# Kernel optimization log

Hardware: AMD Instinct MI355X
Metric: run time of the kernel (lower is better)

Reference implementation:

```python
import jax, jax.numpy as jnp
import numpy as np

NUM_HEADS = 6
EPS = 1e-6

def setup_inputs() -> dict:
    key = jax.random.key(0)
    k1, k2, k3, k4, k5 = jax.random.split(key, 5)
    B, N, C = 8, 1024, 384
    x = jax.random.normal(k1, (B, N, C), dtype=jnp.float32)
    # torch nn.Linear weights stored here as [in, out] for y = x @ W
    w_qkv = jax.random.normal(k2, (C, 3 * C), dtype=jnp.float32) * 0.02
    w_out = jax.random.normal(k3, (C, C), dtype=jnp.float32) * 0.02
    b_out = jax.random.normal(k4, (C,), dtype=jnp.float32) * 0.02
    # non-negative random-walk visitation mask (avg visits per node)
    mask = jax.random.uniform(k5, (N, N), dtype=jnp.float32)
    return {"x": x, "w_qkv": w_qkv, "w_out": w_out, "b_out": b_out, "mask": mask}

def reference(x, w_qkv, w_out, b_out, mask):
    B, N, C = x.shape
    H = NUM_HEADS
    D = C // H
    qkv = x @ w_qkv                                   # [B,N,3C]
    q, k, v = jnp.split(qkv, 3, axis=-1)
    # [B,N,C] -> [B,H,N,D]
    to_heads = lambda t: t.reshape(B, N, H, D).transpose(0, 2, 1, 3)
    q, k, v = to_heads(q), to_heads(k), to_heads(v)
    # feature map: relu(x) + eps
    q = jax.nn.relu(q) + EPS
    k = jax.nn.relu(k) + EPS
    # masked linear kernel: (Phi(Q) Phi(K)^T * mask)
    kernel = jnp.einsum("bhnd,bhmd->bhnm", q, k) * mask  # [B,H,N,N]
    z = 1.0 / (kernel.sum(axis=-1, keepdims=True) + EPS)  # row normalizer
    out = jnp.einsum("bhnm,bhmd->bhnd", kernel, v) * z    # [B,H,N,D]
    out = out.transpose(0, 2, 1, 3).reshape(B, N, C)
    return out @ w_out + b_out
```

## Files before the change

kernel.cpp:

```cpp
#include <hip/hip_runtime.h>
#include <hip/hip_bf16.h>
#include <hip/hip_fp16.h>
#include <stdint.h>

typedef __hip_bfloat16 bf16;
typedef __attribute__((ext_vector_type(8))) short short8;
typedef __attribute__((ext_vector_type(4))) float f32x4;
typedef __attribute__((ext_vector_type(16))) float f32x16;
typedef __attribute__((ext_vector_type(4))) int int4v;
typedef __attribute__((ext_vector_type(4))) unsigned short ushort4v;

#define MFMA16(A,B,C) __builtin_amdgcn_mfma_f32_16x16x32_bf16(A,B,C,0,0,0)
#define MFMA32(A,B,C) __builtin_amdgcn_mfma_f32_32x32x16_bf16(A,B,C,0,0,0)

#define FENCE() asm volatile("" ::: "memory")
#define SBAR()  do { FENCE(); __builtin_amdgcn_s_barrier(); FENCE(); } while (0)
#define WAITVN(N) asm volatile("s_waitcnt vmcnt(" #N ")" ::: "memory")

static __device__ __forceinline__ void g2lds16(const void* g, void* l) {
  __builtin_amdgcn_global_load_lds(
      (__attribute__((address_space(1))) void*)(g),
      (__attribute__((address_space(3))) void*)(l), 16, 0, 0);
}

static __device__ __forceinline__ int swz8(int row, int kc) {
  return row * 8 + (kc ^ (row & 7));
}

static __device__ __forceinline__ unsigned short f2bf_bits(float f) {
  bf16 t = __float2bfloat16(f); unsigned short u; __builtin_memcpy(&u, &t, 2); return u;
}
static __device__ __forceinline__ unsigned short f2h_bits(float f) {
  __half t = __float2half(f); unsigned short u; __builtin_memcpy(&u, &t, 2); return u;
}

template<bool HALFOUT>
static __device__ __forceinline__ void tileT(const float* __restrict__ in,
                                             unsigned short* __restrict__ out,
                                             int R, int C, int tr, int tc, int tid,
                                             float (*tls)[65]) {
  const int rr0 = tid >> 4, c4 = tid & 15;
  #pragma unroll
  for (int rr = 0; rr < 4; ++rr) {
    int r = rr0 + rr * 16;
    float4 v = *(const float4*)(in + (size_t)(tr * 64 + r) * C + tc * 64 + c4 * 4);
    tls[r][c4 * 4 + 0] = v.x; tls[r][c4 * 4 + 1] = v.y;
    tls[r][c4 * 4 + 2] = v.z; tls[r][c4 * 4 + 3] = v.w;
  }
  __syncthreads();
  #pragma unroll
  for (int rr = 0; rr < 4; ++rr) {
    int r2 = rr0 + rr * 16;
    ushort4v o;
    #pragma unroll
    for (int k = 0; k < 4; ++k) {
      float f = tls[c4 * 4 + k][r2];
      o[k] = HALFOUT ? f2h_bits(f) : f2bf_bits(f);
    }
    *(ushort4v*)(out + (size_t)(tc * 64 + r2) * R + tr * 64 + c4 * 4) = o;
  }
}

__global__ __launch_bounds__(256)
void k_prep(const float* __restrict__ x, bf16* __restrict__ xb,
            const float* __restrict__ wqkv, unsigned short* __restrict__ wqkvT,
            const float* __restrict__ wout, unsigned short* __restrict__ woutT,
            const float* __restrict__ mask, unsigned short* __restrict__ maskT) {
  __shared__ float tls[64][65];
  const int bid = blockIdx.x, tid = threadIdx.x;
  if (bid < 768) {
    #pragma unroll
    for (int j = 0; j < 4; ++j) {
      int i = bid * 1024 + j * 256 + tid;
      float4 v = ((const float4*)x)[i];
      bf16* po = xb + (size_t)i * 4;
      po[0] = __float2bfloat16(v.x); po[1] = __float2bfloat16(v.y);
      po[2] = __float2bfloat16(v.z); po[3] = __float2bfloat16(v.w);
    }
  } else if (bid < 876) {
    int tt = bid - 768; tileT<false>(wqkv, wqkvT, 384, 1152, tt / 18, tt % 18, tid, tls);
  } else if (bid < 912) {
    int tt = bid - 876; tileT<false>(wout, woutT, 384, 384, tt / 6, tt % 6, tid, tls);
  } else {
    int tt = bid - 912; tileT<true>(mask, maskT, 1024, 1024, tt / 16, tt % 16, tid, tls);
  }
}

__global__ __launch_bounds__(256, 3)
void k_gemm_qkv(const bf16* __restrict__ A, const bf16* __restrict__ BT,
                bf16* __restrict__ Cb, bf16* __restrict__ vT)
{
  __shared__ __align__(16) bf16 As[128 * 64];
  __shared__ __align__(16) bf16 Bs[96 * 64];
  const int tid = threadIdx.x;
  const int wave = tid >> 6, lane = tid & 63;
  const int lhi = lane >> 4, llo = lane & 15;
  const int wr = wave >> 1, wc = wave & 1;
  const int mBase = blockIdx.x * 128, nBase = blockIdx.y * 96;
  const int K = 384, N = 1152;

  f32x4 acc[4][3] = {};

  for (int kt = 0; kt < K; kt += 64) {
    __syncthreads();
    #pragma unroll
    for (int i = 0; i < 4; ++i) {
      int c = i * 256 + tid;
      int row = c >> 3;
      int kc = (c & 7) ^ (row & 7);
      g2lds16(A + (size_t)(mBase + row) * K + kt + kc * 8, As + (c & ~63) * 8);
    }
    #pragma unroll
    for (int i = 0; i < 3; ++i) {
      int c = i * 256 + tid;
      int row = c >> 3;
      int kc = (c & 7) ^ (row & 7);
      g2lds16(BT + (size_t)(nBase + row) * K + kt + kc * 8, Bs + (c & ~63) * 8);
    }
    __syncthreads();
    for (int kk = 0; kk < 2; ++kk) {
      const int kc = kk * 4 + lhi;
      short8 a[4], b[3];
      #pragma unroll
      for (int mi = 0; mi < 4; ++mi)
        a[mi] = *(const short8*)(As + swz8(wr * 64 + mi * 16 + llo, kc) * 8);
      #pragma unroll
      for (int ni = 0; ni < 3; ++ni)
        b[ni] = *(const short8*)(Bs + swz8(wc * 48 + ni * 16 + llo, kc) * 8);
      #pragma unroll
      for (int mi = 0; mi < 4; ++mi)
        #pragma unroll
        for (int ni = 0; ni < 3; ++ni)
          acc[mi][ni] = MFMA16(a[mi], b[ni], acc[mi][ni]);
    }
  }

  const bool isV = (nBase >= 768);
  #pragma unroll
  for (int mi = 0; mi < 4; ++mi)
    #pragma unroll
    for (int ni = 0; ni < 3; ++ni) {
      const int colbase = nBase + wc * 48 + ni * 16;
      if (!isV) {
        #pragma unroll
        for (int j = 0; j < 4; ++j) {
          int row = mBase + wr * 64 + mi * 16 + lhi * 4 + j;
          int col = colbase + llo;
          float v = fmaxf(acc[mi][ni][j], 0.f) + 1e-6f;
          Cb[(size_t)row * N + col] = __float2bfloat16(v);
        }
      } else {
        int col = colbase + llo;
        int dall = col - 768, hh = dall >> 6, dd = dall & 63;
        int rowg = mBase + wr * 64 + mi * 16 + lhi * 4;
        int bb = rowg >> 10, nloc = rowg & 1023;
        ushort4v pk;
        #pragma unroll
        for (int j = 0; j < 4; ++j) pk[j] = f2bf_bits(acc[mi][ni][j]);
        *(ushort4v*)((unsigned short*)vT + (((size_t)bb * 6 + hh) * 64 + dd) * 1024 + nloc) = pk;
      }
    }
}

__global__ __launch_bounds__(256, 3)
void k_attn(const bf16* __restrict__ qkv,
            const bf16* __restrict__ vT,
            const __half* __restrict__ maskT,
            bf16* __restrict__ out)
{
  __shared__ __align__(16) char smem[49664];
  bf16* KsB = (bf16*)smem;
  bf16* VsB = KsB + 3 * 4096;
  float* OredF = (float*)smem;
  float* zredF = (float*)(smem + 49152);

  const int bid = blockIdx.x;
  const int bh = bid % 48, qt = bid / 48;
  const int b = bh / 6, h = bh - b * 6;
  const int tid = threadIdx.x, wave = tid >> 6, lane = tid & 63;
  const int lq = lane & 31, lh = lane >> 5;
  const int wq = wave & 1, wm = wave >> 1;
  const size_t row0 = (size_t)b * 1024;
  const int qglob = qt * 64 + wq * 32 + lq;

  auto stageKV = [&](int mt, int buf) {
    #pragma unroll
    for (int i = 0; i < 2; ++i) {
      int c = (wave * 2 + i) * 64 + lane;
      int row = c >> 3;
      int kc = (c & 7) ^ (row & 7);
      g2lds16(qkv + (row0 + mt * 64 + row) * 1152 + 384 + h * 64 + kc * 8,
              KsB + buf * 4096 + (c & ~63) * 8);
      g2lds16(vT + ((size_t)bh * 64 + row) * 1024 + mt * 64 + kc * 8,
              VsB + buf * 4096 + (c & ~63) * 8);
    }
  };
  auto loadMask = [&](int mt, __half (&mv)[16]) {
    const int mrow0 = mt * 64 + wm * 32 + 4 * lh;
    #pragma unroll
    for (int g = 0; g < 4; ++g)
      #pragma unroll
      for (int j = 0; j < 4; ++j)
        mv[g * 4 + j] = maskT[(size_t)(mrow0 + 8 * g + j) * 1024 + qglob];
  };

  short8 bq[4];
  {
    const bf16* qp = qkv + (row0 + qglob) * 1152 + h * 64 + lh * 8;
    #pragma unroll
    for (int ks = 0; ks < 4; ++ks) bq[ks] = *(const short8*)(qp + ks * 16);
  }

  f32x16 accO[2] = {};
  float zl = 0.f;

  __half mvA[16], mvB[16];
  stageKV(0, 0);
  loadMask(0, mvA);

  auto iter = [&](int t, __half (&mvUse)[16], __half (&mvPre)[16]) {
    const int bc = t % 3;
    const bf16* Kc = KsB + bc * 4096;
    const bf16* Vc = VsB + bc * 4096;

    if (t < 15) {
      stageKV(t + 1, (t + 1) % 3);
      WAITVN(4);
    } else {
      WAITVN(0);
    }
    asm volatile("s_waitcnt lgkmcnt(0)" ::: "memory");
    SBAR();

    if (t < 15) loadMask(t + 1, mvPre);

    f32x16 st = {};
    #pragma unroll
    for (int ks = 0; ks < 4; ++ks) {
      int row = wm * 32 + lq;
      int cc = (ks * 2 + lh) ^ (row & 7);
      short8 af = *(const short8*)(Kc + (row * 8 + cc) * 8);
      st = MFMA32(af, bq[ks], st);
    }

    float p[16];
    {
      float zp = 0.f;
      #pragma unroll
      for (int r = 0; r < 16; ++r) {
        p[r] = st[r] * __half2float(mvUse[r]);
        zp += p[r];
      }
      zl += zp;
    }
    int u[4][2];
    #pragma unroll
    for (int g = 0; g < 4; ++g)
      #pragma unroll
      for (int c = 0; c < 2; ++c)
        asm("v_cvt_pk_bf16_f32 %0, %1, %2"
            : "=v"(u[g][c]) : "v"(p[4 * g + 2 * c]), "v"(p[4 * g + 2 * c + 1]));

    short8 pa[2];
    #pragma unroll
    for (int ks = 0; ks < 2; ++ks) {
      int A0 = u[2 * ks][0], A0b = u[2 * ks][1];
      int A1 = u[2 * ks + 1][0], A1b = u[2 * ks + 1][1];
      int x0 = __shfl_xor(A0, 32), x1 = __shfl_xor(A0b, 32);
      int y0 = __shfl_xor(A1, 32), y1 = __shfl_xor(A1b, 32);
      int4v iv;
      iv.x = lh ? y0 : A0;
      iv.y = lh ? y1 : A0b;
      iv.z = lh ? A1 : x0;
      iv.w = lh ? A1b : x1;
      pa[ks] = *(short8*)&iv;
    }

    #pragma unroll
    for (int db = 0; db < 2; ++db)
      #pragma unroll
      for (int ks = 0; ks < 2; ++ks) {
        int row = db * 32 + lq;
        int cc = (wm * 4 + ks * 2 + lh) ^ (row & 7);
        short8 vb = *(const short8*)(Vc + (row * 8 + cc) * 8);
        accO[db] = MFMA32(pa[ks], vb, accO[db]);
      }
  };

  #pragma unroll 1
  for (int mt2 = 0; mt2 < 8; ++mt2) {
    iter(2 * mt2,     mvA, mvB);
    iter(2 * mt2 + 1, mvB, mvA);
  }
  __syncthreads();

  zl += __shfl_xor(zl, 32);
  zredF[(wq * 2 + wm) * 32 + lq] = zl;
  if (wm == 1) {
    #pragma unroll
    for (int db = 0; db < 2; ++db)
      #pragma unroll
      for (int r = 0; r < 16; ++r) {
        int q = (r & 3) + 8 * (r >> 2) + 4 * lh;
        OredF[(wq * 32 + q) * 65 + db * 32 + lq] = accO[db][r];
      }
  }
  __syncthreads();
  if (wm == 0) {
    #pragma unroll
    for (int r = 0; r < 16; ++r) {
      int q = (r & 3) + 8 * (r >> 2) + 4 * lh;
      float zt = zredF[wq * 2 * 32 + q] + zredF[(wq * 2 + 1) * 32 + q];
      float zi = 1.f / (zt + 1e-6f);
      int n = qt * 64 + wq * 32 + q;
      size_t orow = (row0 + n) * 384 + h * 64;
      #pragma unroll
      for (int db = 0; db < 2; ++db) {
        float val = (accO[db][r] + OredF[(wq * 32 + q) * 65 + db * 32 + lq]) * zi;
        out[orow + db * 32 + lq] = __float2bfloat16(val);
      }
    }
  }
}

__global__ __launch_bounds__(256, 3)
void k_gemm_out(const bf16* __restrict__ A, const bf16* __restrict__ BT,
                float* __restrict__ Cf, const float* __restrict__ bias)
{
  __shared__ __align__(16) bf16 As[64 * 64];
  __shared__ __align__(16) bf16 Bs[64 * 64];
  const int tid = threadIdx.x;
  const int wave = tid >> 6, lane = tid & 63;
  const int lq = lane & 31, lh = lane >> 5;
  const int wr = wave >> 1, wc = wave & 1;
  const int mBase = blockIdx.x * 64, nBase = blockIdx.y * 64;
  const int N = 384, K = 384;

  f32x16 acc = {};
  for (int kt = 0; kt < K; kt += 64) {
    __syncthreads();
    #pragma unroll
    for (int i = 0; i < 2; ++i) {
      int c = (wave * 2 + i) * 64 + lane;
      int row = c >> 3;
      int kc = (c & 7) ^ (row & 7);
      g2lds16(A  + (size_t)(mBase + row) * K + kt + kc * 8, As + (c & ~63) * 8);
      g2lds16(BT + (size_t)(nBase + row) * K + kt + kc * 8, Bs + (c & ~63) * 8);
    }
    __syncthreads();
    #pragma unroll
    for (int ks = 0; ks < 4; ++ks) {
      int ra = wr * 32 + lq, rb = wc * 32 + lq;
      short8 a = *(const short8*)(As + (ra * 8 + ((ks * 2 + lh) ^ (ra & 7))) * 8);
      short8 b = *(const short8*)(Bs + (rb * 8 + ((ks * 2 + lh) ^ (rb & 7))) * 8);
      acc = MFMA32(a, b, acc);
    }
  }
  #pragma unroll
  for (int r = 0; r < 16; ++r) {
    int row = mBase + wr * 32 + (r & 3) + 8 * (r >> 2) + 4 * lh;
    int col = nBase + wc * 32 + lq;
    Cf[(size_t)row * N + col] = acc[r] + bias[col];
  }
}

extern "C" void kernel_launch(void* const* d_in, const int* in_sizes, int n_in,
                              void* d_out, int out_size, void* d_ws, size_t ws_size,
                              hipStream_t stream) {
  (void)in_sizes; (void)n_in; (void)out_size; (void)ws_size;
  const float* x    = (const float*)d_in[0];
  const float* wqkv = (const float*)d_in[1];
  const float* wout = (const float*)d_in[2];
  const float* bout = (const float*)d_in[3];
  const float* mask = (const float*)d_in[4];
  float* outp = (float*)d_out;

  char* ws = (char*)d_ws;
  bf16*  xb    = (bf16*)(ws);
  bf16*  wqkvT = (bf16*)(ws + 6291456);
  bf16*  woutT = (bf16*)(ws + 7176192);
  bf16*  qkvb  = (bf16*)(ws + 7471104);
  bf16*  vTb   = (bf16*)(ws + 26345472);
  bf16*  ab    = (bf16*)(ws + 32636928);
  __half* maskT = (__half*)(ws + 38928384);

  k_prep<<<dim3(1168), dim3(256), 0, stream>>>(
      x, xb, wqkv, (unsigned short*)wqkvT, wout, (unsigned short*)woutT,
      mask, (unsigned short*)maskT);

  k_gemm_qkv<<<dim3(64, 12), dim3(256), 0, stream>>>(xb, wqkvT, qkvb, vTb);
  k_attn<<<dim3(768), dim3(256), 0, stream>>>(qkvb, vTb, maskT, ab);
  k_gemm_out<<<dim3(128, 6), dim3(256), 0, stream>>>(ab, woutT, outp, bout);
}
```

Before: 57.03 us.

## Triple-buffer QKV GEMM K-tiles with async global-to-LDS prefetch

Restructures the QKV projection GEMM main loop from a single 64-wide K tile with two barriers per step into a three-stage ring of 32-wide K tiles. The next tile is prefetched with global_load_lds while the current one is consumed, using a vmcnt wait and one barrier per step. The goal is to hide global load latency behind MFMA work. It doubles the iteration count, adopts a 4-way XOR swizzle, and leaves some lanes idle in the B staging.

Measured after the change: 59.69 us. 1.05x slower.

```diff
diff --git a/kernel.cpp b/kernel.cpp
--- a/kernel.cpp
+++ b/kernel.cpp
@@ -16,6 +16,7 @@
 #define FENCE() asm volatile("" ::: "memory")
 #define SBAR()  do { FENCE(); __builtin_amdgcn_s_barrier(); FENCE(); } while (0)
 #define WAITVN(N) asm volatile("s_waitcnt vmcnt(" #N ")" ::: "memory")
+#define LGKM0() asm volatile("s_waitcnt lgkmcnt(0)" ::: "memory")
 
 static __device__ __forceinline__ void g2lds16(const void* g, void* l) {
   __builtin_amdgcn_global_load_lds(
@@ -90,8 +91,8 @@
 void k_gemm_qkv(const bf16* __restrict__ A, const bf16* __restrict__ BT,
                 bf16* __restrict__ Cb, bf16* __restrict__ vT)
 {
-  __shared__ __align__(16) bf16 As[128 * 64];
-  __shared__ __align__(16) bf16 Bs[96 * 64];
+  __shared__ __align__(16) bf16 AsB[3][128 * 32];
+  __shared__ __align__(16) bf16 BsB[3][96 * 32];
   const int tid = threadIdx.x;
   const int wave = tid >> 6, lane = tid & 63;
   const int lhi = lane >> 4, llo = lane & 15;
@@ -99,40 +100,63 @@
   const int mBase = blockIdx.x * 128, nBase = blockIdx.y * 96;
   const int K = 384, N = 1152;
 
+  auto stage = [&](int kt, int buf) {
+    #pragma unroll
+    for (int i = 0; i < 2; ++i) {
+      int c0 = wave * 128 + i * 64;
+      int c = c0 + lane;
+      int row = c >> 2;
+      int kc = (c & 3) ^ (row & 3);
+      g2lds16(A + (size_t)(mBase + row) * K + kt + kc * 8, AsB[buf] + c0 * 8);
+    }
+    {
+      int c0 = wave * 96;
+      int c = c0 + lane;
+      int row = c >> 2;
+      int kc = (c & 3) ^ (row & 3);
+      g2lds16(BT + (size_t)(nBase + row) * K + kt + kc * 8, BsB[buf] + c0 * 8);
+    }
+    {
+      int c0 = wave * 96 + 64;
+      int c = c0 + lane;
+      int row = c >> 2;
+      int kc = (c & 3) ^ (row & 3);
+      if (lane < 32)
+        g2lds16(BT + (size_t)(nBase + row) * K + kt + kc * 8, BsB[buf] + c0 * 8);
+    }
+  };
+
   f32x4 acc[4][3] = {};
-
-  for (int kt = 0; kt < K; kt += 64) {
-    __syncthreads();
-    #pragma unroll
-    for (int i = 0; i < 4; ++i) {
-      int c = i * 256 + tid;
-      int row = c >> 3;
-      int kc = (c & 7) ^ (row & 7);
-      g2lds16(A + (size_t)(mBase + row) * K + kt + kc * 8, As + (c & ~63) * 8);
-    }
-    #pragma unroll
-    for (int i = 0; i < 3; ++i) {
-      int c = i * 256 + tid;
-      int row = c >> 3;
-      int kc = (c & 7) ^ (row & 7);
-      g2lds16(BT + (size_t)(nBase + row) * K + kt + kc * 8, Bs + (c & ~63) * 8);
-    }
-    __syncthreads();
-    for (int kk = 0; kk < 2; ++kk) {
-      const int kc = kk * 4 + lhi;
-      short8 a[4], b[3];
-      #pragma unroll
-      for (int mi = 0; mi < 4; ++mi)
-        a[mi] = *(const short8*)(As + swz8(wr * 64 + mi * 16 + llo, kc) * 8);
+  stage(0, 0);
+
+  #pragma unroll 1
+  for (int t = 0; t < 12; ++t) {
+    const int bc = t % 3;
+    if (t < 11) {
+      stage((t + 1) * 32, (t + 1) % 3);
+      WAITVN(4);
+    } else {
+      WAITVN(0);
+    }
+    LGKM0();
+    SBAR();
+
+    short8 a[4], b[3];
+    #pragma unroll
+    for (int mi = 0; mi < 4; ++mi) {
+      int r = wr * 64 + mi * 16 + llo;
+      a[mi] = *(const short8*)(AsB[bc] + (r * 4 + (lhi ^ (r & 3))) * 8);
+    }
+    #pragma unroll
+    for (int ni = 0; ni < 3; ++ni) {
+      int r = wc * 48 + ni * 16 + llo;
+      b[ni] = *(const short8*)(BsB[bc] + (r * 4 + (lhi ^ (r & 3))) * 8);
+    }
+    #pragma unroll
+    for (int mi = 0; mi < 4; ++mi)
       #pragma unroll
       for (int ni = 0; ni < 3; ++ni)
-        b[ni] = *(const short8*)(Bs + swz8(wc * 48 + ni * 16 + llo, kc) * 8);
-      #pragma unroll
-      for (int mi = 0; mi < 4; ++mi)
-        #pragma unroll
-        for (int ni = 0; ni < 3; ++ni)
-          acc[mi][ni] = MFMA16(a[mi], b[ni], acc[mi][ni]);
-    }
+        acc[mi][ni] = MFMA16(a[mi], b[ni], acc[mi][ni]);
   }
 
   const bool isV = (nBase >= 768);
@@ -229,7 +253,7 @@
     } else {
       WAITVN(0);
     }
-    asm volatile("s_waitcnt lgkmcnt(0)" ::: "memory");
+    LGKM0();
     SBAR();
 
     if (t < 15) loadMask(t + 1, mvPre);
```
